# Kernel tuning notes

Measured on AMD Instinct MI355X. Metric: run time of the kernel, lower is better.

## Reference

```python
import jax, jax.numpy as jnp
import numpy as np

N_NODES = 100000
N_FEAT = 128
HIDDEN = 32
HEADS = 4
N_CLASSES = 40
N_EDGES = 1600000
NEG_SLOPE = 0.2


def gat_conv(x, src, dst, W, att_src, att_dst, bias):
    """PyG-style GATConv (concat=True, eval mode, self-loops already in src/dst).
    x: [N, Fin], W: [Fin, H*C], att_src/att_dst: [H, C], bias: [H*C].
    """
    N = x.shape[0]
    H, C = att_src.shape
    h = (x @ W).reshape(N, H, C)                       # [N, H, C]
    a_src = jnp.einsum('nhc,hc->nh', h, att_src)       # [N, H]
    a_dst = jnp.einsum('nhc,hc->nh', h, att_dst)       # [N, H]
    e = a_src[src] + a_dst[dst]                        # [E, H]
    e = jnp.where(e > 0, e, NEG_SLOPE * e)             # leaky_relu(0.2)
    # segment softmax over incoming edges of each destination node
    e_max = jax.ops.segment_max(e, dst, num_segments=N)
    e = jnp.exp(e - e_max[dst])
    denom = jax.ops.segment_sum(e, dst, num_segments=N)
    alpha = e / (denom[dst] + 1e-16)                   # [E, H]
    msg = alpha[:, :, None] * h[src]                   # [E, H, C]
    out = jax.ops.segment_sum(msg, dst, num_segments=N)  # [N, H, C]
    return out.reshape(N, H * C) + bias


def setup_inputs() -> dict:
    key = jax.random.key(0)
    ks = jax.random.split(key, 10)
    s = 0.1
    x = jax.random.normal(ks[0], (N_NODES, N_FEAT), dtype=jnp.float32)
    edge_index = jax.random.randint(ks[1], (2, N_EDGES), 0, N_NODES, dtype=jnp.int32)
    W1 = jax.random.normal(ks[2], (N_FEAT, HEADS * HIDDEN), dtype=jnp.float32) * s
    att_src1 = jax.random.normal(ks[3], (HEADS, HIDDEN), dtype=jnp.float32) * s
    att_dst1 = jax.random.normal(ks[4], (HEADS, HIDDEN), dtype=jnp.float32) * s
    b1 = jnp.zeros((HEADS * HIDDEN,), dtype=jnp.float32)
    W2 = jax.random.normal(ks[5], (HEADS * HIDDEN, HEADS * HIDDEN), dtype=jnp.float32) * s
    att_src2 = jax.random.normal(ks[6], (HEADS, HIDDEN), dtype=jnp.float32) * s
    att_dst2 = jax.random.normal(ks[7], (HEADS, HIDDEN), dtype=jnp.float32) * s
    b2 = jnp.zeros((HEADS * HIDDEN,), dtype=jnp.float32)
    Wc = jax.random.normal(ks[8], (HEADS * HIDDEN, N_CLASSES), dtype=jnp.float32) * s
    bc = jnp.zeros((N_CLASSES,), dtype=jnp.float32)
    return {"x": x, "edge_index": edge_index, "W1": W1, "att_src1": att_src1,
            "att_dst1": att_dst1, "b1": b1, "W2": W2, "att_src2": att_src2,
            "att_dst2": att_dst2, "b2": b2, "Wc": Wc, "bc": bc}


def reference(x, edge_index, W1, att_src1, att_dst1, b1, W2, att_src2, att_dst2, b2, Wc, bc):
    N = x.shape[0]
    loops = jnp.arange(N, dtype=edge_index.dtype)
    src = jnp.concatenate([edge_index[0], loops])  # PyG add_self_loops=True
    dst = jnp.concatenate([edge_index[1], loops])
    h = gat_conv(x, src, dst, W1, att_src1, att_dst1, b1)
    h = jax.nn.relu(h)  # dropout p=0.5 inactive in eval
    h = gat_conv(h, src, dst, W2, att_src2, att_dst2, b2)
    h = jax.nn.relu(h)  # dropout p=0.6 inactive in eval
    return h @ Wc + bc
```

## Files before the change

### kernel.cpp

```cpp
#include <hip/hip_runtime.h>

#define NN   100000
#define NE   1600000
#define BSH  9
#define BSZ  512
#define NBK  196
#define TA   8192
#define NBA  196
#define SCAP 96
#define CAP2 9216
#define NBG  782
#define NPREP 6

typedef _Float16 half_t;
typedef __attribute__((ext_vector_type(2))) _Float16 f16x2;
typedef __attribute__((ext_vector_type(4))) _Float16 f16x4;
typedef __attribute__((ext_vector_type(8))) _Float16 f16x8;
typedef __attribute__((ext_vector_type(4))) float    f32x4;

__global__ __launch_bounds__(256) void k_front(const float* __restrict__ X, const float* __restrict__ W1,
                                               const float* __restrict__ atts, const float* __restrict__ attd,
                                               half_t* __restrict__ H, float* __restrict__ asrc,
                                               float* __restrict__ adst,
                                               const float* __restrict__ W2, const float* __restrict__ Wc,
                                               half_t* __restrict__ WT2, half_t* __restrict__ WTc,
                                               const int* __restrict__ src, const int* __restrict__ dst,
                                               unsigned int* __restrict__ bpk, int* __restrict__ bh) {
  __shared__ __align__(16) char smem[36864];
  int t = threadIdx.x;
  int bid = blockIdx.x;

  if (bid >= NBG + NPREP) {
    int hb = bid - NBG - NPREP;
    int* hist  = (int*)smem;
    int* hscan = hist + NBK;
    int* cnt   = hscan + NBK;
    int* ssc   = cnt + NBK;
    unsigned int* staged = (unsigned int*)(ssc + 256);
    int e0 = hb * TA;
    if (t < NBK) { hist[t] = 0; cnt[t] = 0; }
    __syncthreads();
#pragma unroll
    for (int i = 0; i < TA / 256; i++) {
      int e = e0 + t + i * 256;
      if (e < NE) atomicAdd(&hist[dst[e] >> BSH], 1);
    }
    __syncthreads();
    {
      int v = (t < NBK) ? hist[t] : 0;
      int x = v;
      ssc[t] = x;
      for (int off = 1; off < 256; off <<= 1) {
        __syncthreads();
        int y = (t >= off) ? ssc[t - off] : 0;
        __syncthreads();
        x += y;
        ssc[t] = x;
      }
      if (t < NBK) hscan[t] = x - v;
    }
    __syncthreads();
#pragma unroll
    for (int i = 0; i < TA / 256; i++) {
      int e = e0 + t + i * 256;
      if (e < NE) {
        int d = dst[e];
        int bk = d >> BSH;
        int pos = hscan[bk] + atomicAdd(&cnt[bk], 1);
        staged[pos] = ((unsigned int)src[e] << BSH) | (unsigned int)(d & (BSZ - 1));
      }
    }
    __syncthreads();
    int wave = t >> 6, lane = t & 63;
    for (int bk = wave; bk < NBK; bk += 4) {
      int c = hist[bk];
      int cw = min(c, SCAP);
      size_t base = ((size_t)bk * NBA + hb) * SCAP;
      int lo = hscan[bk];
      for (int j = lane; j < cw; j += 64) bpk[base + j] = staged[lo + j];
      if (lane == 0) bh[bk * NBA + hb] = cw;
    }
    return;
  }

  if (bid >= NBG) {
    int b = bid - NBG;
    float (*tile)[65] = (float(*)[65])smem;
    const float* W;
    half_t* WT;
    int k0, n0, N, NTr;
    if (b < 4) { W = W2; WT = WT2; k0 = (b >> 1) * 64; n0 = (b & 1) * 64; N = 128; NTr = 128; }
    else       { int bb = b - 4; W = Wc; WT = WTc; k0 = bb * 64; n0 = 0; N = 40; NTr = 48; }
    int col = t & 63, r4 = t >> 6;
#pragma unroll
    for (int i = 0; i < 16; i++) {
      int row = r4 * 16 + i;
      float v = 0.f;
      if (n0 + col < N) v = W[(size_t)(k0 + row) * N + n0 + col];
      tile[row][col] = v;
    }
    __syncthreads();
#pragma unroll
    for (int i = 0; i < 16; i++) {
      int nrow = r4 * 16 + i;
      if (n0 + nrow < NTr) WT[(size_t)(n0 + nrow) * 128 + k0 + col] = (half_t)tile[col][nrow];
    }
    return;
  }

  half_t* Xt = (half_t*)smem;
  half_t* Wt = Xt + 128 * 40;
  int wave = t >> 6, lane = t & 63;
  int l15 = lane & 15, quad = lane >> 4;
  int rb = bid * 128;

  f32x4 acc[2][8];
#pragma unroll
  for (int rt = 0; rt < 2; rt++)
#pragma unroll
    for (int ct = 0; ct < 8; ct++) acc[rt][ct] = (f32x4){0.f, 0.f, 0.f, 0.f};

  for (int k0 = 0; k0 < 128; k0 += 32) {
    __syncthreads();
#pragma unroll
    for (int i = 0; i < 4; i++) {
      int lin = i * 256 + t;
      int row = lin >> 3;
      int c4 = (lin & 7) * 4;
      float4 v = make_float4(0.f, 0.f, 0.f, 0.f);
      int gr = rb + row;
      if (gr < NN) v = *(const float4*)(X + (size_t)gr * 128 + k0 + c4);
      f16x4 hv;
      hv[0] = (half_t)v.x; hv[1] = (half_t)v.y; hv[2] = (half_t)v.z; hv[3] = (half_t)v.w;
      *(f16x4*)(Xt + row * 40 + c4) = hv;
    }
#pragma unroll
    for (int i = 0; i < 4; i++) {
      int lin = i * 256 + t;
      int kr = lin >> 5;
      int n4 = (lin & 31) * 4;
      float4 v = *(const float4*)(W1 + (size_t)(k0 + kr) * 128 + n4);
      Wt[(n4 + 0) * 40 + kr] = (half_t)v.x;
      Wt[(n4 + 1) * 40 + kr] = (half_t)v.y;
      Wt[(n4 + 2) * 40 + kr] = (half_t)v.z;
      Wt[(n4 + 3) * 40 + kr] = (half_t)v.w;
    }
    __syncthreads();

    f16x8 a0 = *(const f16x8*)(Xt + (wave * 32 + l15) * 40 + quad * 8);
    f16x8 a1 = *(const f16x8*)(Xt + (wave * 32 + 16 + l15) * 40 + quad * 8);
#pragma unroll
    for (int ct = 0; ct < 8; ct++) {
      f16x8 b = *(const f16x8*)(Wt + (ct * 16 + l15) * 40 + quad * 8);
      acc[0][ct] = __builtin_amdgcn_mfma_f32_16x16x32_f16(a0, b, acc[0][ct], 0, 0, 0);
      acc[1][ct] = __builtin_amdgcn_mfma_f32_16x16x32_f16(a1, b, acc[1][ct], 0, 0, 0);
    }
  }

#pragma unroll
  for (int rt = 0; rt < 2; rt++) {
    int rbase = rb + wave * 32 + rt * 16 + quad * 4;
#pragma unroll
    for (int reg = 0; reg < 4; reg++) {
      int row = rbase + reg;
      if (row < NN) {
#pragma unroll
        for (int ct = 0; ct < 8; ct++) {
          H[(size_t)row * 128 + ct * 16 + l15] = (half_t)acc[rt][ct][reg];
        }
      }
    }
  }

  float s_lo[4], s_hi[4], d_lo[4], d_hi[4];
#pragma unroll
  for (int h = 0; h < 4; h++) {
    s_lo[h] = atts[h * 32 + l15];
    s_hi[h] = atts[h * 32 + 16 + l15];
    d_lo[h] = attd[h * 32 + l15];
    d_hi[h] = attd[h * 32 + 16 + l15];
  }
#pragma unroll
  for (int rt = 0; rt < 2; rt++) {
    float ps[4][4], pd[4][4];
#pragma unroll
    for (int reg = 0; reg < 4; reg++)
#pragma unroll
      for (int h = 0; h < 4; h++) {
        ps[reg][h] = acc[rt][2 * h][reg] * s_lo[h] + acc[rt][2 * h + 1][reg] * s_hi[h];
        pd[reg][h] = acc[rt][2 * h][reg] * d_lo[h] + acc[rt][2 * h + 1][reg] * d_hi[h];
      }
#pragma unroll
    for (int m = 1; m < 16; m <<= 1) {
#pragma unroll
      for (int reg = 0; reg < 4; reg++)
#pragma unroll
        for (int h = 0; h < 4; h++) {
          ps[reg][h] += __shfl_xor(ps[reg][h], m, 64);
          pd[reg][h] += __shfl_xor(pd[reg][h], m, 64);
        }
    }
    float vs = 0.f, vd = 0.f;
#pragma unroll
    for (int reg = 0; reg < 4; reg++)
#pragma unroll
      for (int h = 0; h < 4; h++) {
        if (l15 == reg * 4 + h) { vs = ps[reg][h]; vd = pd[reg][h]; }
      }
    int row = rb + wave * 32 + rt * 16 + quad * 4 + (l15 >> 2);
    int h = l15 & 3;
    if (row < NN) {
      asrc[row * 4 + h] = vs;
      adst[row * 4 + h] = vd;
    }
  }
}

__global__ __launch_bounds__(256) void k_binB(const unsigned int* __restrict__ bpk,
                                              const int* __restrict__ bh,
                                              int* __restrict__ sbeg, int* __restrict__ send,
                                              int* __restrict__ adj) {
  __shared__ int lhist[BSZ];
  __shared__ int lscan[BSZ];
  __shared__ int lcur[BSZ];
  __shared__ int ssc[256];
  __shared__ int carr[NBA];
  __shared__ unsigned int staged[CAP2];
  int b = blockIdx.x;
  int t = threadIdx.x;
  int nbeg = b << BSH;
  int nloc = min(BSZ, NN - nbeg);
  int adjb = b * CAP2;
  if (t < NBA) carr[t] = bh[b * NBA + t];
  lhist[2 * t] = (2 * t < nloc) ? 1 : 0;
  lhist[2 * t + 1] = (2 * t + 1 < nloc) ? 1 : 0;
  lcur[2 * t] = 1;
  lcur[2 * t + 1] = 1;
  __syncthreads();
  int wave = t >> 6, lane = t & 63;
  for (int a = wave; a < NBA; a += 4) {
    int c = carr[a];
    size_t base = ((size_t)b * NBA + a) * SCAP;
    for (int j = lane; j < c; j += 64) atomicAdd(&lhist[bpk[base + j] & (BSZ - 1)], 1);
  }
  __syncthreads();
  {
    int v0 = lhist[2 * t], v1 = lhist[2 * t + 1];
    int s2 = v0 + v1;
    int x = s2;
    ssc[t] = x;
    for (int off = 1; off < 256; off <<= 1) {
      __syncthreads();
      int y = (t >= off) ? ssc[t - off] : 0;
      __syncthreads();
      x += y;
      ssc[t] = x;
    }
    int ex = x - s2;
    lscan[2 * t] = ex;
    lscan[2 * t + 1] = ex + v0;
  }
  __syncthreads();
  int total = lscan[BSZ - 1] + lhist[BSZ - 1];
#pragma unroll
  for (int u = 0; u < 2; u++) {
    int i = t + u * 256;
    if (i < nloc) {
      int bg = adjb + lscan[i];
      sbeg[nbeg + i] = bg;
      send[nbeg + i] = bg + lhist[i];
      staged[lscan[i]] = (unsigned int)(nbeg + i);
    }
  }
  __syncthreads();
  for (int a = wave; a < NBA; a += 4) {
    int c = carr[a];
    size_t base = ((size_t)b * NBA + a) * SCAP;
    for (int j = lane; j < c; j += 64) {
      unsigned int v = bpk[base + j];
      int dl = v & (BSZ - 1);
      int idx = lscan[dl] + atomicAdd(&lcur[dl], 1);
      if (idx < CAP2) staged[idx] = v >> BSH;
    }
  }
  __syncthreads();
  int lim = min(total, CAP2);
  for (int i = t; i < lim; i += 256) adj[adjb + i] = (int)staged[i];
}

__global__ __launch_bounds__(256) void k_agg(const half_t* __restrict__ H, const int* __restrict__ sbeg,
                                             const int* __restrict__ send, const int* __restrict__ adj,
                                             const float* __restrict__ asrc, const float* __restrict__ adst,
                                             const float* __restrict__ bias, half_t* __restrict__ out) {
  int n = blockIdx.x * 4 + (threadIdx.x >> 6);
  if (n >= NN) return;
  int lane = threadIdx.x & 63;
  int sub = lane & 7;
  int g = lane >> 3;
  int head = sub >> 1;
  float ad = adst[(size_t)n * 4 + head];
  float acc[16];
#pragma unroll
  for (int j = 0; j < 16; j++) acc[j] = 0.f;
  float wsum = 0.f;
  int beg = sbeg[n], end = send[n];
  int i = beg + g;
  int s = 0;
  float a = 0.f;
  if (i < end) {
    s = adj[i];
    a = asrc[(size_t)s * 4 + head];
  }
  while (i < end) {
    int inext = i + 8;
    int sn = 0;
    float an = 0.f;
    if (inext < end) {
      sn = adj[inext];
      an = asrc[(size_t)sn * 4 + head];
    }
    float ev = a + ad;
    ev = (ev > 0.f) ? ev : 0.2f * ev;
    float w = __expf(ev);
    const f16x8* hp = (const f16x8*)(H + (size_t)s * 128 + sub * 16);
    f16x8 h0 = hp[0], h1 = hp[1];
    wsum += w;
#pragma unroll
    for (int j = 0; j < 8; j++) acc[j] += w * (float)h0[j];
#pragma unroll
    for (int j = 0; j < 8; j++) acc[8 + j] += w * (float)h1[j];
    s = sn; a = an; i = inext;
  }
#pragma unroll
  for (int m = 8; m < 64; m <<= 1) {
    wsum += __shfl_xor(wsum, m, 64);
#pragma unroll
    for (int j = 0; j < 16; j++) acc[j] += __shfl_xor(acc[j], m, 64);
  }
  float scale = 1.0f / (wsum + 1e-16f);
  float o0 = acc[0], o1 = acc[1];
#pragma unroll
  for (int r = 1; r < 8; r++) {
    if (g == r) { o0 = acc[2 * r]; o1 = acc[2 * r + 1]; }
  }
  int ch = sub * 16 + g * 2;
  o0 = fmaxf(o0 * scale + bias[ch], 0.f);
  o1 = fmaxf(o1 * scale + bias[ch + 1], 0.f);
  f16x2 o;
  o[0] = (half_t)o0;
  o[1] = (half_t)o1;
  *(f16x2*)(out + (size_t)n * 128 + ch) = o;
}

__global__ __launch_bounds__(256) void k_gemm_att(const half_t* __restrict__ X, const half_t* __restrict__ WT,
                                                  const float* __restrict__ atts, const float* __restrict__ attd,
                                                  half_t* __restrict__ H, float* __restrict__ asrc,
                                                  float* __restrict__ adst) {
  __shared__ __align__(16) half_t Xt[128 * 40];
  __shared__ __align__(16) half_t Wt[128 * 40];
  int t = threadIdx.x;
  int wave = t >> 6, lane = t & 63;
  int l15 = lane & 15, quad = lane >> 4;
  int rb = blockIdx.x * 128;

  f32x4 acc[2][8];
#pragma unroll
  for (int rt = 0; rt < 2; rt++)
#pragma unroll
    for (int ct = 0; ct < 8; ct++) acc[rt][ct] = (f32x4){0.f, 0.f, 0.f, 0.f};

  for (int k0 = 0; k0 < 128; k0 += 32) {
    __syncthreads();
#pragma unroll
    for (int i = 0; i < 2; i++) {
      int lin = i * 256 + t;
      int row = lin >> 2;
      int c8 = (lin & 3) * 8;
      f16x8 hv = (f16x8)(half_t)0;
      int gr = rb + row;
      if (gr < NN) hv = *(const f16x8*)(X + (size_t)gr * 128 + k0 + c8);
      *(f16x8*)(Xt + row * 40 + c8) = hv;
    }
#pragma unroll
    for (int i = 0; i < 2; i++) {
      int lin = i * 256 + t;
      int row = lin >> 2;
      int c8 = (lin & 3) * 8;
      *(f16x8*)(Wt + row * 40 + c8) = *(const f16x8*)(WT + (size_t)row * 128 + k0 + c8);
    }
    __syncthreads();

    f16x8 a0 = *(const f16x8*)(Xt + (wave * 32 + l15) * 40 + quad * 8);
    f16x8 a1 = *(const f16x8*)(Xt + (wave * 32 + 16 + l15) * 40 + quad * 8);
#pragma unroll
    for (int ct = 0; ct < 8; ct++) {
      f16x8 b = *(const f16x8*)(Wt + (ct * 16 + l15) * 40 + quad * 8);
      acc[0][ct] = __builtin_amdgcn_mfma_f32_16x16x32_f16(a0, b, acc[0][ct], 0, 0, 0);
      acc[1][ct] = __builtin_amdgcn_mfma_f32_16x16x32_f16(a1, b, acc[1][ct], 0, 0, 0);
    }
  }

#pragma unroll
  for (int rt = 0; rt < 2; rt++) {
    int rbase = rb + wave * 32 + rt * 16 + quad * 4;
#pragma unroll
    for (int reg = 0; reg < 4; reg++) {
      int row = rbase + reg;
      if (row < NN) {
#pragma unroll
        for (int ct = 0; ct < 8; ct++) {
          H[(size_t)row * 128 + ct * 16 + l15] = (half_t)acc[rt][ct][reg];
        }
      }
    }
  }

  float s_lo[4], s_hi[4], d_lo[4], d_hi[4];
#pragma unroll
  for (int h = 0; h < 4; h++) {
    s_lo[h] = atts[h * 32 + l15];
    s_hi[h] = atts[h * 32 + 16 + l15];
    d_lo[h] = attd[h * 32 + l15];
    d_hi[h] = attd[h * 32 + 16 + l15];
  }
#pragma unroll
  for (int rt = 0; rt < 2; rt++) {
    float ps[4][4], pd[4][4];
#pragma unroll
    for (int reg = 0; reg < 4; reg++)
#pragma unroll
      for (int h = 0; h < 4; h++) {
        ps[reg][h] = acc[rt][2 * h][reg] * s_lo[h] + acc[rt][2 * h + 1][reg] * s_hi[h];
        pd[reg][h] = acc[rt][2 * h][reg] * d_lo[h] + acc[rt][2 * h + 1][reg] * d_hi[h];
      }
#pragma unroll
    for (int m = 1; m < 16; m <<= 1) {
#pragma unroll
      for (int reg = 0; reg < 4; reg++)
#pragma unroll
        for (int h = 0; h < 4; h++) {
          ps[reg][h] += __shfl_xor(ps[reg][h], m, 64);
          pd[reg][h] += __shfl_xor(pd[reg][h], m, 64);
        }
    }
    float vs = 0.f, vd = 0.f;
#pragma unroll
    for (int reg = 0; reg < 4; reg++)
#pragma unroll
      for (int h = 0; h < 4; h++) {
        if (l15 == reg * 4 + h) { vs = ps[reg][h]; vd = pd[reg][h]; }
      }
    int row = rb + wave * 32 + rt * 16 + quad * 4 + (l15 >> 2);
    int h = l15 & 3;
    if (row < NN) {
      asrc[row * 4 + h] = vs;
      adst[row * 4 + h] = vd;
    }
  }
}

__global__ __launch_bounds__(256) void k_classifier(const half_t* __restrict__ Hf, const half_t* __restrict__ WTc,
                                                    const float* __restrict__ bc, float* __restrict__ out) {
  __shared__ __align__(16) half_t Xt[128 * 40];
  __shared__ __align__(16) half_t Wt[48 * 40];
  int t = threadIdx.x;
  int wave = t >> 6, lane = t & 63;
  int l15 = lane & 15, quad = lane >> 4;
  int rb = blockIdx.x * 128;

  f32x4 acc[2][3];
#pragma unroll
  for (int rt = 0; rt < 2; rt++)
#pragma unroll
    for (int ct = 0; ct < 3; ct++) acc[rt][ct] = (f32x4){0.f, 0.f, 0.f, 0.f};

  for (int k0 = 0; k0 < 128; k0 += 32) {
    __syncthreads();
#pragma unroll
    for (int i = 0; i < 2; i++) {
      int lin = i * 256 + t;
      int row = lin >> 2;
      int c8 = (lin & 3) * 8;
      f16x8 hv = (f16x8)(half_t)0;
      int gr = rb + row;
      if (gr < NN) hv = *(const f16x8*)(Hf + (size_t)gr * 128 + k0 + c8);
      *(f16x8*)(Xt + row * 40 + c8) = hv;
    }
    if (t < 192) {
      int row = t >> 2;
      int c8 = (t & 3) * 8;
      *(f16x8*)(Wt + row * 40 + c8) = *(const f16x8*)(WTc + (size_t)row * 128 + k0 + c8);
    }
    __syncthreads();

    f16x8 a0 = *(const f16x8*)(Xt + (wave * 32 + l15) * 40 + quad * 8);
    f16x8 a1 = *(const f16x8*)(Xt + (wave * 32 + 16 + l15) * 40 + quad * 8);
#pragma unroll
    for (int ct = 0; ct < 3; ct++) {
      f16x8 b = *(const f16x8*)(Wt + (ct * 16 + l15) * 40 + quad * 8);
      acc[0][ct] = __builtin_amdgcn_mfma_f32_16x16x32_f16(a0, b, acc[0][ct], 0, 0, 0);
      acc[1][ct] = __builtin_amdgcn_mfma_f32_16x16x32_f16(a1, b, acc[1][ct], 0, 0, 0);
    }
  }

#pragma unroll
  for (int rt = 0; rt < 2; rt++) {
#pragma unroll
    for (int ct = 0; ct < 3; ct++) {
      int col = ct * 16 + l15;
      if (col < 40) {
        float bv = bc[col];
#pragma unroll
        for (int reg = 0; reg < 4; reg++) {
          int row = rb + wave * 32 + rt * 16 + quad * 4 + reg;
          if (row < NN) out[(size_t)row * 40 + col] = acc[rt][ct][reg] + bv;
        }
      }
    }
  }
}


extern "C" void kernel_launch(void* const* d_in, const int* in_sizes, int n_in,
                              void* d_out, int out_size, void* d_ws, size_t ws_size,
                              hipStream_t stream) {
  const float* x   = (const float*)d_in[0];
  const int*   ei  = (const int*)d_in[1];
  const float* W1  = (const float*)d_in[2];
  const float* as1 = (const float*)d_in[3];
  const float* ad1 = (const float*)d_in[4];
  const float* b1  = (const float*)d_in[5];
  const float* W2  = (const float*)d_in[6];
  const float* as2 = (const float*)d_in[7];
  const float* ad2 = (const float*)d_in[8];
  const float* b2  = (const float*)d_in[9];
  const float* Wc  = (const float*)d_in[10];
  const float* bc  = (const float*)d_in[11];
  float* out = (float*)d_out;

  const int* esrc = ei;
  const int* edst = ei + NE;

  char* w = (char*)d_ws;
  auto alloc = [&](size_t bytes) {
    void* p = (void*)w;
    w += (bytes + 255) & ~(size_t)255;
    return p;
  };
  half_t* A   = (half_t*)alloc(sizeof(half_t) * (size_t)NN * 128);
  half_t* B   = (half_t*)alloc(sizeof(half_t) * (size_t)NN * 128);
  float* asrc = (float*)alloc(sizeof(float) * (size_t)NN * 4);
  float* adst = (float*)alloc(sizeof(float) * (size_t)NN * 4);
  int* sbeg   = (int*)alloc(sizeof(int) * NN);
  int* send   = (int*)alloc(sizeof(int) * NN);
  unsigned int* bpk = (unsigned int*)alloc(sizeof(unsigned int) * (size_t)NBK * NBA * SCAP);
  int* bh     = (int*)alloc(sizeof(int) * NBK * NBA);
  int* adj    = (int*)alloc(sizeof(int) * (size_t)NBK * CAP2);
  half_t* WT2 = (half_t*)alloc(sizeof(half_t) * 128 * 128);
  half_t* WTc = (half_t*)alloc(sizeof(half_t) * 48 * 128);

  k_front<<<NBG + NPREP + NBA, 256, 0, stream>>>(x, W1, as1, ad1, A, asrc, adst,
                                                 W2, Wc, WT2, WTc, esrc, edst, bpk, bh);
  k_binB<<<NBK, 256, 0, stream>>>(bpk, bh, sbeg, send, adj);

  k_agg<<<(NN + 3) / 4, 256, 0, stream>>>(A, sbeg, send, adj, asrc, adst, b1, B);

  k_gemm_att<<<(NN + 127) / 128, 256, 0, stream>>>(B, WT2, as2, ad2, A, asrc, adst);
  k_agg<<<(NN + 3) / 4, 256, 0, stream>>>(A, sbeg, send, adj, asrc, adst, b2, B);

  k_classifier<<<(NN + 127) / 128, 256, 0, stream>>>(B, WTc, bc, out);
}
```

Measured before the change: 393.8 us.

## Fold attention vectors into GEMM weights as extra MFMA columns; shrink bin tiles

Precomputes W·att_src and W·att_dst as 8 extra weight columns, so each GEMM gets a ninth MFMA column tile that yields the attention logits directly. This replaces the per-row shuffle reductions in both the first-layer and second-layer GEMM epilogues. It also changes the edge-binning parameters to more, smaller tiles (TA 4096, 391 histogram blocks, SCAP 64), which cuts shared memory and adds parallelism in binning. The cost is extra MFMA work, logits formed from fp16-rounded folded weights, and a tighter per-tile capacity that could overflow on skewed inputs.

```diff
diff --git a/kernel.cpp b/kernel.cpp
--- a/kernel.cpp
+++ b/kernel.cpp
@@ -5,12 +5,12 @@
 #define BSH  9
 #define BSZ  512
 #define NBK  196
-#define TA   8192
-#define NBA  196
-#define SCAP 96
+#define TA   4096
+#define NBA  391
+#define SCAP 64
 #define CAP2 9216
 #define NBG  782
-#define NPREP 6
+#define NPREP 7
 
 typedef _Float16 half_t;
 typedef __attribute__((ext_vector_type(2))) _Float16 f16x2;
@@ -23,10 +23,11 @@
                                                half_t* __restrict__ H, float* __restrict__ asrc,
                                                float* __restrict__ adst,
                                                const float* __restrict__ W2, const float* __restrict__ Wc,
+                                               const float* __restrict__ atts2, const float* __restrict__ attd2,
                                                half_t* __restrict__ WT2, half_t* __restrict__ WTc,
                                                const int* __restrict__ src, const int* __restrict__ dst,
                                                unsigned int* __restrict__ bpk, int* __restrict__ bh) {
-  __shared__ __align__(16) char smem[36864];
+  __shared__ __align__(16) char smem[21760];
   int t = threadIdx.x;
   int bid = blockIdx.x;
 
@@ -85,6 +86,25 @@
 
   if (bid >= NBG) {
     int b = bid - NBG;
+    if (b == 6) {
+      int e = t >> 5, kr = t & 31, h = e & 3;
+      const float* att = ((e < 4) ? atts2 : attd2) + h * 32;
+#pragma unroll
+      for (int u = 0; u < 4; u++) {
+        int k = u * 32 + kr;
+        const float* wrow = W2 + (size_t)k * 128 + h * 32;
+        float s = 0.f;
+#pragma unroll
+        for (int c = 0; c < 32; c += 4) {
+          float4 wv = *(const float4*)(wrow + c);
+          float4 av = *(const float4*)(att + c);
+          s += wv.x * av.x + wv.y * av.y + wv.z * av.z + wv.w * av.w;
+        }
+        WT2[(size_t)(128 + e) * 128 + k] = (half_t)s;
+      }
+      for (int u = t; u < 8 * 128; u += 256) WT2[(size_t)136 * 128 + u] = (half_t)0.f;
+      return;
+    }
     float (*tile)[65] = (float(*)[65])smem;
     const float* W;
     half_t* WT;
@@ -114,11 +134,13 @@
   int l15 = lane & 15, quad = lane >> 4;
   int rb = bid * 128;
 
-  f32x4 acc[2][8];
+  for (int u = t; u < 8 * 40; u += 256) Wt[136 * 40 + u] = (half_t)0.f;
+
+  f32x4 acc[2][9];
 #pragma unroll
   for (int rt = 0; rt < 2; rt++)
 #pragma unroll
-    for (int ct = 0; ct < 8; ct++) acc[rt][ct] = (f32x4){0.f, 0.f, 0.f, 0.f};
+    for (int ct = 0; ct < 9; ct++) acc[rt][ct] = (f32x4){0.f, 0.f, 0.f, 0.f};
 
   for (int k0 = 0; k0 < 128; k0 += 32) {
     __syncthreads();
@@ -145,12 +167,25 @@
       Wt[(n4 + 2) * 40 + kr] = (half_t)v.z;
       Wt[(n4 + 3) * 40 + kr] = (half_t)v.w;
     }
+    {
+      int e = t >> 5, kr = t & 31, h = e & 3;
+      const float* att = ((e < 4) ? atts : attd) + h * 32;
+      const float* wrow = W1 + (size_t)(k0 + kr) * 128 + h * 32;
+      float s = 0.f;
+#pragma unroll
+      for (int c = 0; c < 32; c += 4) {
+        float4 wv = *(const float4*)(wrow + c);
+        float4 av = *(const float4*)(att + c);
+        s += wv.x * av.x + wv.y * av.y + wv.z * av.z + wv.w * av.w;
+      }
+      Wt[(128 + e) * 40 + kr] = (half_t)s;
+    }
     __syncthreads();
 
     f16x8 a0 = *(const f16x8*)(Xt + (wave * 32 + l15) * 40 + quad * 8);
     f16x8 a1 = *(const f16x8*)(Xt + (wave * 32 + 16 + l15) * 40 + quad * 8);
 #pragma unroll
-    for (int ct = 0; ct < 8; ct++) {
+    for (int ct = 0; ct < 9; ct++) {
       f16x8 b = *(const f16x8*)(Wt + (ct * 16 + l15) * 40 + quad * 8);
       acc[0][ct] = __builtin_amdgcn_mfma_f32_16x16x32_f16(a0, b, acc[0][ct], 0, 0, 0);
       acc[1][ct] = __builtin_amdgcn_mfma_f32_16x16x32_f16(a1, b, acc[1][ct], 0, 0, 0);
@@ -168,50 +203,12 @@
         for (int ct = 0; ct < 8; ct++) {
           H[(size_t)row * 128 + ct * 16 + l15] = (half_t)acc[rt][ct][reg];
         }
-      }
-    }
-  }
-
-  float s_lo[4], s_hi[4], d_lo[4], d_hi[4];
-#pragma unroll
-  for (int h = 0; h < 4; h++) {
-    s_lo[h] = atts[h * 32 + l15];
-    s_hi[h] = atts[h * 32 + 16 + l15];
-    d_lo[h] = attd[h * 32 + l15];
-    d_hi[h] = attd[h * 32 + 16 + l15];
-  }
-#pragma unroll
-  for (int rt = 0; rt < 2; rt++) {
-    float ps[4][4], pd[4][4];
-#pragma unroll
-    for (int reg = 0; reg < 4; reg++)
-#pragma unroll
-      for (int h = 0; h < 4; h++) {
-        ps[reg][h] = acc[rt][2 * h][reg] * s_lo[h] + acc[rt][2 * h + 1][reg] * s_hi[h];
-        pd[reg][h] = acc[rt][2 * h][reg] * d_lo[h] + acc[rt][2 * h + 1][reg] * d_hi[h];
-      }
-#pragma unroll
-    for (int m = 1; m < 16; m <<= 1) {
-#pragma unroll
-      for (int reg = 0; reg < 4; reg++)
-#pragma unroll
-        for (int h = 0; h < 4; h++) {
-          ps[reg][h] += __shfl_xor(ps[reg][h], m, 64);
-          pd[reg][h] += __shfl_xor(pd[reg][h], m, 64);
+        if (l15 < 8) {
+          float v = acc[rt][8][reg];
+          if (l15 < 4) asrc[row * 4 + l15] = v;
+          else         adst[row * 4 + (l15 - 4)] = v;
         }
-    }
-    float vs = 0.f, vd = 0.f;
-#pragma unroll
-    for (int reg = 0; reg < 4; reg++)
-#pragma unroll
-      for (int h = 0; h < 4; h++) {
-        if (l15 == reg * 4 + h) { vs = ps[reg][h]; vd = pd[reg][h]; }
-      }
-    int row = rb + wave * 32 + rt * 16 + quad * 4 + (l15 >> 2);
-    int h = l15 & 3;
-    if (row < NN) {
-      asrc[row * 4 + h] = vs;
-      adst[row * 4 + h] = vd;
+      }
     }
   }
 }
@@ -231,7 +228,7 @@
   int nbeg = b << BSH;
   int nloc = min(BSZ, NN - nbeg);
   int adjb = b * CAP2;
-  if (t < NBA) carr[t] = bh[b * NBA + t];
+  for (int u = t; u < NBA; u += 256) carr[u] = bh[b * NBA + u];
   lhist[2 * t] = (2 * t < nloc) ? 1 : 0;
   lhist[2 * t + 1] = (2 * t + 1 < nloc) ? 1 : 0;
   lcur[2 * t] = 1;
@@ -353,21 +350,20 @@
 }
 
 __global__ __launch_bounds__(256) void k_gemm_att(const half_t* __restrict__ X, const half_t* __restrict__ WT,
-                                                  const float* __restrict__ atts, const float* __restrict__ attd,
                                                   half_t* __restrict__ H, float* __restrict__ asrc,
                                                   float* __restrict__ adst) {
   __shared__ __align__(16) half_t Xt[128 * 40];
-  __shared__ __align__(16) half_t Wt[128 * 40];
+  __shared__ __align__(16) half_t Wt[144 * 40];
   int t = threadIdx.x;
   int wave = t >> 6, lane = t & 63;
   int l15 = lane & 15, quad = lane >> 4;
   int rb = blockIdx.x * 128;
 
-  f32x4 acc[2][8];
+  f32x4 acc[2][9];
 #pragma unroll
   for (int rt = 0; rt < 2; rt++)
 #pragma unroll
-    for (int ct = 0; ct < 8; ct++) acc[rt][ct] = (f32x4){0.f, 0.f, 0.f, 0.f};
+    for (int ct = 0; ct < 9; ct++) acc[rt][ct] = (f32x4){0.f, 0.f, 0.f, 0.f};
 
   for (int k0 = 0; k0 < 128; k0 += 32) {
     __syncthreads();
@@ -382,18 +378,20 @@
       *(f16x8*)(Xt + row * 40 + c8) = hv;
     }
 #pragma unroll
-    for (int i = 0; i < 2; i++) {
+    for (int i = 0; i < 3; i++) {
       int lin = i * 256 + t;
-      int row = lin >> 2;
-      int c8 = (lin & 3) * 8;
-      *(f16x8*)(Wt + row * 40 + c8) = *(const f16x8*)(WT + (size_t)row * 128 + k0 + c8);
+      if (lin < 576) {
+        int row = lin >> 2;
+        int c8 = (lin & 3) * 8;
+        *(f16x8*)(Wt + row * 40 + c8) = *(const f16x8*)(WT + (size_t)row * 128 + k0 + c8);
+      }
     }
     __syncthreads();
 
     f16x8 a0 = *(const f16x8*)(Xt + (wave * 32 + l15) * 40 + quad * 8);
     f16x8 a1 = *(const f16x8*)(Xt + (wave * 32 + 16 + l15) * 40 + quad * 8);
 #pragma unroll
-    for (int ct = 0; ct < 8; ct++) {
+    for (int ct = 0; ct < 9; ct++) {
       f16x8 b = *(const f16x8*)(Wt + (ct * 16 + l15) * 40 + quad * 8);
       acc[0][ct] = __builtin_amdgcn_mfma_f32_16x16x32_f16(a0, b, acc[0][ct], 0, 0, 0);
       acc[1][ct] = __builtin_amdgcn_mfma_f32_16x16x32_f16(a1, b, acc[1][ct], 0, 0, 0);
@@ -411,50 +409,12 @@
         for (int ct = 0; ct < 8; ct++) {
           H[(size_t)row * 128 + ct * 16 + l15] = (half_t)acc[rt][ct][reg];
         }
-      }
-    }
-  }
-
-  float s_lo[4], s_hi[4], d_lo[4], d_hi[4];
-#pragma unroll
-  for (int h = 0; h < 4; h++) {
-    s_lo[h] = atts[h * 32 + l15];
-    s_hi[h] = atts[h * 32 + 16 + l15];
-    d_lo[h] = attd[h * 32 + l15];
-    d_hi[h] = attd[h * 32 + 16 + l15];
-  }
-#pragma unroll
-  for (int rt = 0; rt < 2; rt++) {
-    float ps[4][4], pd[4][4];
-#pragma unroll
-    for (int reg = 0; reg < 4; reg++)
-#pragma unroll
-      for (int h = 0; h < 4; h++) {
-        ps[reg][h] = acc[rt][2 * h][reg] * s_lo[h] + acc[rt][2 * h + 1][reg] * s_hi[h];
-        pd[reg][h] = acc[rt][2 * h][reg] * d_lo[h] + acc[rt][2 * h + 1][reg] * d_hi[h];
-      }
-#pragma unroll
-    for (int m = 1; m < 16; m <<= 1) {
-#pragma unroll
-      for (int reg = 0; reg < 4; reg++)
-#pragma unroll
-        for (int h = 0; h < 4; h++) {
-          ps[reg][h] += __shfl_xor(ps[reg][h], m, 64);
-          pd[reg][h] += __shfl_xor(pd[reg][h], m, 64);
+        if (l15 < 8) {
+          float v = acc[rt][8][reg];
+          if (l15 < 4) asrc[row * 4 + l15] = v;
+          else         adst[row * 4 + (l15 - 4)] = v;
         }
-    }
-    float vs = 0.f, vd = 0.f;
-#pragma unroll
-    for (int reg = 0; reg < 4; reg++)
-#pragma unroll
-      for (int h = 0; h < 4; h++) {
-        if (l15 == reg * 4 + h) { vs = ps[reg][h]; vd = pd[reg][h]; }
-      }
-    int row = rb + wave * 32 + rt * 16 + quad * 4 + (l15 >> 2);
-    int h = l15 & 3;
-    if (row < NN) {
-      asrc[row * 4 + h] = vs;
-      adst[row * 4 + h] = vd;
+      }
     }
   }
 }
@@ -556,16 +516,16 @@
   unsigned int* bpk = (unsigned int*)alloc(sizeof(unsigned int) * (size_t)NBK * NBA * SCAP);
   int* bh     = (int*)alloc(sizeof(int) * NBK * NBA);
   int* adj    = (int*)alloc(sizeof(int) * (size_t)NBK * CAP2);
-  half_t* WT2 = (half_t*)alloc(sizeof(half_t) * 128 * 128);
+  half_t* WT2 = (half_t*)alloc(sizeof(half_t) * 144 * 128);
   half_t* WTc = (half_t*)alloc(sizeof(half_t) * 48 * 128);
 
   k_front<<<NBG + NPREP + NBA, 256, 0, stream>>>(x, W1, as1, ad1, A, asrc, adst,
-                                                 W2, Wc, WT2, WTc, esrc, edst, bpk, bh);
+                                                 W2, Wc, as2, ad2, WT2, WTc, esrc, edst, bpk, bh);
   k_binB<<<NBK, 256, 0, stream>>>(bpk, bh, sbeg, send, adj);
 
   k_agg<<<(NN + 3) / 4, 256, 0, stream>>>(A, sbeg, send, adj, asrc, adst, b1, B);
 
-  k_gemm_att<<<(NN + 127) / 128, 256, 0, stream>>>(B, WT2, as2, ad2, A, asrc, adst);
+  k_gemm_att<<<(NN + 127) / 128, 256, 0, stream>>>(B, WT2, A, asrc, adst);
   k_agg<<<(NN + 3) / 4, 256, 0, stream>>>(A, sbeg, send, adj, asrc, adst, b2, B);
 
   k_classifier<<<(NN + 127) / 128, 256, 0, stream>>>(B, WTc, bc, out);
```

After: 410.5 us. 1.04x slower.
